# Performance work log

Measured on AMD Instinct MI355X. Metric: run time of the kernel, lower is better.

The kernel has to match this reference:

```python
import jax, jax.numpy as jnp
import numpy as np
import math
from jax import lax

B, T, C = 32, 512, 256
NL, NH, FF = 2, 4, 1024
DH = C // NH
NFREQ = 64   # n_even//2 for d_model=256 (even dims interleave sin/cos)
N_ODD = 128  # odd dims carry learned ramp a*t+b
MIN_P, MAX_P = 4.0, 10000.0


def setup_inputs() -> dict:
    key = jax.random.key(0)
    ks = jax.random.split(key, 16)
    def nrm(k, shape, s=0.02):
        return (jax.random.normal(k, shape) * s).astype(jnp.float32)
    x = jax.random.normal(ks[0], (B, T, C), jnp.float32)
    # strictly increasing normalized timestamps
    dts = jax.random.uniform(ks[1], (B, T), jnp.float32) * 0.02 + 1e-3
    ts = jnp.cumsum(dts, axis=1)
    return {
        "x": x, "ts": ts,
        "gru_Wih": nrm(ks[2], (3 * C, C)), "gru_Whh": nrm(ks[3], (3 * C, C)),
        "gru_bih": jnp.zeros((3 * C,), jnp.float32), "gru_bhh": jnp.zeros((3 * C,), jnp.float32),
        "ode_W": nrm(ks[4], (C, 4 * C)), "ode_b": jnp.zeros((C,), jnp.float32),
        "norm_ode_g": jnp.ones((C,), jnp.float32), "norm_ode_b": jnp.zeros((C,), jnp.float32),
        "norm_gru_g": jnp.ones((C,), jnp.float32), "norm_gru_b": jnp.zeros((C,), jnp.float32),
        "film_W": nrm(ks[5], (2 * C, C)), "film_b": jnp.zeros((2 * C,), jnp.float32),
        "te_a": nrm(ks[6], (N_ODD,), 1.0), "te_b": nrm(ks[7], (N_ODD,), 0.1),
        "qkv_W": nrm(ks[8], (NL, 3 * C, C)), "qkv_b": jnp.zeros((NL, 3 * C), jnp.float32),
        "out_W": nrm(ks[9], (NL, C, C)), "out_b": jnp.zeros((NL, C), jnp.float32),
        "ln1_g": jnp.ones((NL, C), jnp.float32), "ln1_b": jnp.zeros((NL, C), jnp.float32),
        "ln2_g": jnp.ones((NL, C), jnp.float32), "ln2_b": jnp.zeros((NL, C), jnp.float32),
        "ff1_W": nrm(ks[10], (NL, FF, C)), "ff1_b": jnp.zeros((NL, FF), jnp.float32),
        "ff2_W": nrm(ks[11], (NL, C, FF)), "ff2_b": jnp.zeros((NL, C), jnp.float32),
        "lnf_g": jnp.ones((C,), jnp.float32), "lnf_b": jnp.zeros((C,), jnp.float32),
    }


def _ln(x, g, b, eps=1e-5):
    m = x.mean(-1, keepdims=True)
    v = ((x - m) ** 2).mean(-1, keepdims=True)
    return (x - m) / jnp.sqrt(v + eps) * g + b


def _forward(x, ts, gru_Wih, gru_Whh, gru_bih, gru_bhh, ode_W, ode_b,
             norm_ode_g, norm_ode_b, norm_gru_g, norm_gru_b, film_W, film_b,
             te_a, te_b, qkv_W, qkv_b, out_W, out_b, ln1_g, ln1_b, ln2_g, ln2_b,
             ff1_W, ff1_b, ff2_W, ff2_b, lnf_g, lnf_b):
    Bx, Tx, Cx = x.shape

    def gru(xi, h):  # PyTorch GRUCell math
        gi = xi @ gru_Wih.T + gru_bih
        gh = h @ gru_Whh.T + gru_bhh
        ir, iz, inn = jnp.split(gi, 3, -1)
        hr, hz, hn = jnp.split(gh, 3, -1)
        r = jax.nn.sigmoid(ir + hr)
        z = jax.nn.sigmoid(iz + hz)
        n = jnp.tanh(inn + r * hn)
        return (1.0 - z) * n + z * h

    def step(h, inp):  # RK4 ODE jump + GRU jump per event
        xi, xp, dt = inp  # (B,C),(B,C),(B,1)
        dx = (xi - xp) / dt
        def f(hh):
            return jnp.tanh(jnp.concatenate([hh, xi, xp, dx], -1) @ ode_W.T + ode_b)
        k1 = f(h)
        k2 = f(h + 0.5 * dt * k1)
        k3 = f(h + 0.5 * dt * k2)
        k4 = f(h + dt * k3)
        h = h + dt / 6.0 * (k1 + 2.0 * k2 + 2.0 * k3 + k4)
        h = _ln(h, norm_ode_g, norm_ode_b)
        h = _ln(gru(xi, h), norm_gru_g, norm_gru_b)
        return h, h

    h0 = _ln(gru(x[:, 0], jnp.zeros((Bx, Cx), x.dtype)), norm_gru_g, norm_gru_b)
    xs = (x[:, 1:].swapaxes(0, 1), x[:, :-1].swapaxes(0, 1),
          (ts[:, 1:] - ts[:, :-1])[..., None].swapaxes(0, 1))
    _, ys = lax.scan(step, h0, xs)
    h = jnp.concatenate([h0[None], ys], 0).swapaxes(0, 1)  # (B,T,C)

    # FiLM params from hidden states
    gb = jax.nn.silu(h) @ film_W.T + film_b
    gamma, beta = jnp.split(gb, 2, -1)

    # TimeHybridEncoding: even dims interleaved sin/cos, odd dims learned ramp
    freqs = jnp.exp(-jnp.linspace(0.0, math.log(MAX_P / MIN_P), NFREQ)) * (2.0 * math.pi / MIN_P)
    phase = ts[..., None] * freqs  # (B,T,NFREQ)
    sc = jnp.stack([jnp.sin(phase), jnp.cos(phase)], -1).reshape(Bx, Tx, 2 * NFREQ)
    ramp = ts[..., None] * te_a + te_b  # (B,T,N_ODD)
    tme = jnp.zeros((Bx, Tx, Cx), x.dtype)
    tme = tme.at[..., 0::2].set(sc).at[..., 1::2].set(ramp)
    tme = (1.0 + gamma) * tme + beta

    # Pre-LN TransformerEncoder (eval mode: dropout off), relu FFN, final LN
    H = h + tme
    scale = 1.0 / jnp.sqrt(jnp.float32(DH))
    for l in range(NL):
        a = _ln(H, ln1_g[l], ln1_b[l])
        qkv = a @ qkv_W[l].T + qkv_b[l]
        q, k, v = jnp.split(qkv, 3, -1)
        q = q.reshape(Bx, Tx, NH, DH).transpose(0, 2, 1, 3)
        k = k.reshape(Bx, Tx, NH, DH).transpose(0, 2, 1, 3)
        v = v.reshape(Bx, Tx, NH, DH).transpose(0, 2, 1, 3)
        att = jax.nn.softmax(jnp.einsum('bhqd,bhkd->bhqk', q, k) * scale, axis=-1)
        o = jnp.einsum('bhqk,bhkd->bhqd', att, v).transpose(0, 2, 1, 3).reshape(Bx, Tx, Cx)
        H = H + o @ out_W[l].T + out_b[l]
        f2 = _ln(H, ln2_g[l], ln2_b[l])
        H = H + jax.nn.relu(f2 @ ff1_W[l].T + ff1_b[l]) @ ff2_W[l].T + ff2_b[l]
    return _ln(H, lnf_g, lnf_b)


def reference(x, ts, gru_Wih, gru_Whh, gru_bih, gru_bhh, ode_W, ode_b,
              norm_ode_g, norm_ode_b, norm_gru_g, norm_gru_b, film_W, film_b,
              te_a, te_b, qkv_W, qkv_b, out_W, out_b, ln1_g, ln1_b, ln2_g, ln2_b,
              ff1_W, ff1_b, ff2_W, ff2_b, lnf_g, lnf_b):
    return _forward(x, ts, gru_Wih, gru_Whh, gru_bih, gru_bhh, ode_W, ode_b,
                    norm_ode_g, norm_ode_b, norm_gru_g, norm_gru_b, film_W, film_b,
                    te_a, te_b, qkv_W, qkv_b, out_W, out_b, ln1_g, ln1_b, ln2_g, ln2_b,
                    ff1_W, ff1_b, ff2_W, ff2_b, lnf_g, lnf_b)
```

## Files before the change

### kernel.cpp

```cpp
#include <hip/hip_runtime.h>
#include <hip/hip_bf16.h>
#include <math.h>

typedef long long i64;

__device__ __forceinline__ float2 blockSum2_256(float a, float b, float* red) {
#pragma unroll
  for (int off = 32; off; off >>= 1) {
    a += __shfl_xor(a, off, 64);
    b += __shfl_xor(b, off, 64);
  }
  __syncthreads();
  if ((threadIdx.x & 63) == 0) {
    int w = threadIdx.x >> 6;
    red[w * 2 + 0] = a;
    red[w * 2 + 1] = b;
  }
  __syncthreads();
  return make_float2(red[0] + red[2] + red[4] + red[6],
                     red[1] + red[3] + red[5] + red[7]);
}

__device__ __forceinline__ float lnVal(float v, float g, float b, float* red) {
  float2 s = blockSum2_256(v, v * v, red);
  float mean = s.x * (1.0f / 256.0f);
  float var = s.y * (1.0f / 256.0f) - mean * mean;
  var = fmaxf(var, 0.0f);
  return (v - mean) * rsqrtf(var + 1e-5f) * g + b;
}

__device__ __forceinline__ void waveRed2d(double& a, double& b) {
#pragma unroll
  for (int off = 32; off; off >>= 1) {
    a += __shfl_xor(a, off, 64);
    b += __shfl_xor(b, off, 64);
  }
}

template <typename ACCT>
__global__ __launch_bounds__(256)
void gemm_nt_t(const float* __restrict__ A, int lda,
               const float* __restrict__ W, int ldw,
               const float* __restrict__ bias,
               const float* add,
               float* C, int ldc,
               int M, int N, int K, int relu)
{
  __shared__ float As[16][68];
  __shared__ float Ws[16][68];
  const int tid = threadIdx.x;
  const int tx = tid & 15, ty = tid >> 4;
  const int m0 = blockIdx.y * 64, n0 = blockIdx.x * 64;
  const int lrow = tid >> 2, lk = (tid & 3) << 2;
  ACCT acc[4][4] = {};
  for (int k0 = 0; k0 < K; k0 += 16) {
    float4 av = make_float4(0.f, 0.f, 0.f, 0.f);
    if (m0 + lrow < M) av = *(const float4*)(A + (i64)(m0 + lrow) * lda + k0 + lk);
    float4 wv = *(const float4*)(W + (i64)(n0 + lrow) * ldw + k0 + lk);
    As[lk + 0][lrow] = av.x; As[lk + 1][lrow] = av.y;
    As[lk + 2][lrow] = av.z; As[lk + 3][lrow] = av.w;
    Ws[lk + 0][lrow] = wv.x; Ws[lk + 1][lrow] = wv.y;
    Ws[lk + 2][lrow] = wv.z; Ws[lk + 3][lrow] = wv.w;
    __syncthreads();
#pragma unroll
    for (int kk = 0; kk < 16; ++kk) {
      ACCT a0 = (ACCT)As[kk][ty * 4 + 0], a1 = (ACCT)As[kk][ty * 4 + 1];
      ACCT a2 = (ACCT)As[kk][ty * 4 + 2], a3 = (ACCT)As[kk][ty * 4 + 3];
      ACCT b0 = (ACCT)Ws[kk][tx * 4 + 0], b1 = (ACCT)Ws[kk][tx * 4 + 1];
      ACCT b2 = (ACCT)Ws[kk][tx * 4 + 2], b3 = (ACCT)Ws[kk][tx * 4 + 3];
      acc[0][0] += a0 * b0; acc[0][1] += a0 * b1; acc[0][2] += a0 * b2; acc[0][3] += a0 * b3;
      acc[1][0] += a1 * b0; acc[1][1] += a1 * b1; acc[1][2] += a1 * b2; acc[1][3] += a1 * b3;
      acc[2][0] += a2 * b0; acc[2][1] += a2 * b1; acc[2][2] += a2 * b2; acc[2][3] += a2 * b3;
      acc[3][0] += a3 * b0; acc[3][1] += a3 * b1; acc[3][2] += a3 * b2; acc[3][3] += a3 * b3;
    }
    __syncthreads();
  }
#pragma unroll
  for (int i = 0; i < 4; ++i) {
    int m = m0 + ty * 4 + i;
    if (m >= M) continue;
#pragma unroll
    for (int j = 0; j < 4; ++j) {
      int n = n0 + tx * 4 + j;
      ACCT v = acc[i][j];
      if (bias) v += (ACCT)bias[n];
      if (relu) v = v > (ACCT)0 ? v : (ACCT)0;
      if (add) v += (ACCT)add[(i64)m * ldc + n];
      C[(i64)m * ldc + n] = (float)v;
    }
  }
}

__global__ __launch_bounds__(256)
void gemm128(const float* __restrict__ A, int lda,
             const float* __restrict__ W, int ldw,
             const float* __restrict__ bias,
             const float* add,
             float* C, int ldc,
             int K, int relu)
{
  __shared__ float As[16][132];
  __shared__ float Ws[16][132];
  const int tid = threadIdx.x;
  const int tx = tid & 15, ty = tid >> 4;
  const int m0 = blockIdx.y * 128, n0 = blockIdx.x * 128;
  const int lrow = tid >> 1;
  const int lk = (tid & 1) * 8;
  float acc[8][8] = {};
  for (int k0 = 0; k0 < K; k0 += 16) {
    const float* ap = A + (i64)(m0 + lrow) * lda + k0 + lk;
    const float* wp = W + (i64)(n0 + lrow) * ldw + k0 + lk;
    float4 av0 = *(const float4*)(ap);
    float4 av1 = *(const float4*)(ap + 4);
    float4 wv0 = *(const float4*)(wp);
    float4 wv1 = *(const float4*)(wp + 4);
    __syncthreads();
    As[lk + 0][lrow] = av0.x; As[lk + 1][lrow] = av0.y;
    As[lk + 2][lrow] = av0.z; As[lk + 3][lrow] = av0.w;
    As[lk + 4][lrow] = av1.x; As[lk + 5][lrow] = av1.y;
    As[lk + 6][lrow] = av1.z; As[lk + 7][lrow] = av1.w;
    Ws[lk + 0][lrow] = wv0.x; Ws[lk + 1][lrow] = wv0.y;
    Ws[lk + 2][lrow] = wv0.z; Ws[lk + 3][lrow] = wv0.w;
    Ws[lk + 4][lrow] = wv1.x; Ws[lk + 5][lrow] = wv1.y;
    Ws[lk + 6][lrow] = wv1.z; Ws[lk + 7][lrow] = wv1.w;
    __syncthreads();
#pragma unroll
    for (int kk = 0; kk < 16; ++kk) {
      float4 a0 = *(const float4*)&As[kk][ty * 4];
      float4 a1 = *(const float4*)&As[kk][64 + ty * 4];
      float4 b0 = *(const float4*)&Ws[kk][tx * 4];
      float4 b1 = *(const float4*)&Ws[kk][64 + tx * 4];
      float a[8] = {a0.x, a0.y, a0.z, a0.w, a1.x, a1.y, a1.z, a1.w};
      float bb[8] = {b0.x, b0.y, b0.z, b0.w, b1.x, b1.y, b1.z, b1.w};
#pragma unroll
      for (int i = 0; i < 8; ++i)
#pragma unroll
        for (int j = 0; j < 8; ++j)
          acc[i][j] = fmaf(a[i], bb[j], acc[i][j]);
    }
  }
#pragma unroll
  for (int i = 0; i < 8; ++i) {
    int m = m0 + ((i < 4) ? (ty * 4 + i) : (64 + ty * 4 + (i - 4)));
#pragma unroll
    for (int g = 0; g < 2; ++g) {
      int n = n0 + g * 64 + tx * 4;
      float v[4];
#pragma unroll
      for (int j = 0; j < 4; ++j) {
        float vv = acc[i][g * 4 + j];
        if (bias) vv += bias[n + j];
        if (relu) vv = fmaxf(vv, 0.f);
        if (add) vv += add[(i64)m * ldc + n + j];
        v[j] = vv;
      }
      *(float4*)(C + (i64)m * ldc + n) = make_float4(v[0], v[1], v[2], v[3]);
    }
  }
}

__global__ __launch_bounds__(256)
void pack_weights(const float* __restrict__ odeW, const float* __restrict__ Whh,
                  float* __restrict__ W4h, float* __restrict__ W4hh)
{
  int idx = blockIdx.x * 256 + threadIdx.x;
  if (idx < 65536) {
    int j = idx >> 8, k = idx & 255;
    W4h[((k >> 2) << 10) + (j << 2) + (k & 3)] = odeW[j * 1024 + k];
  } else {
    int t = idx - 65536;
    int j3 = t >> 8, k = t & 255;
    W4hh[(k >> 2) * 3072 + (j3 << 2) + (k & 3)] = Whh[j3 * 256 + k];
  }
}

__global__ __launch_bounds__(256)
void pack_rowsums(const float* __restrict__ odeW, const float* __restrict__ Whh,
                  const float* __restrict__ ngg, const float* __restrict__ ngb,
                  const float* __restrict__ nog, const float* __restrict__ nob,
                  double* __restrict__ Sd)
{
  int r = blockIdx.x * 256 + threadIdx.x;
  if (r < 256) {
    double s1 = 0.0, s0 = 0.0;
    for (int k = 0; k < 256; ++k) {
      double w = (double)odeW[r * 1024 + k];
      s1 += w * (double)ngg[k];
      s0 += w * (double)ngb[k];
    }
    Sd[r] = s1; Sd[256 + r] = s0;
  } else {
    int j3 = r - 256;
    double s1 = 0.0, s0 = 0.0;
    for (int k = 0; k < 256; ++k) {
      double w = (double)Whh[j3 * 256 + k];
      s1 += w * (double)nog[k];
      s0 += w * (double)nob[k];
    }
    Sd[512 + j3] = s1; Sd[1280 + j3] = s0;
  }
}

__global__ __launch_bounds__(256)
void dx_kernel(const float* __restrict__ x, const float* __restrict__ ts,
               float* __restrict__ dx)
{
  i64 row = blockIdx.x;
  int c = threadIdx.x;
  int t = (int)(row & 511);
  float v = 0.0f;
  if (t > 0) {
    double dt = (double)ts[row] - (double)ts[row - 1];
    v = (float)(((double)x[row * 256 + c] - (double)x[(row - 1) * 256 + c]) / dt);
  }
  dx[row * 256 + c] = v;
}

__global__ __launch_bounds__(256)
void silu_kernel(const float* __restrict__ in, float* __restrict__ out)
{
  i64 i = (i64)blockIdx.x * 256 + threadIdx.x;
  float v = in[i];
  out[i] = v / (1.0f + __expf(-v));
}

__global__ __launch_bounds__(256)
void fill_kernel(float* __restrict__ out, float v)
{
  i64 i = (i64)blockIdx.x * 256 + threadIdx.x;
  out[i] = v;
}

__device__ __forceinline__ float dot64s(const float* __restrict__ W, int kq, int j,
                                        const float* __restrict__ v)
{
  float a0 = 0.f, a1 = 0.f, a2 = 0.f, a3 = 0.f;
#pragma unroll
  for (int m4 = 0; m4 < 16; ++m4) {
    float4 w = *(const float4*)(W + (((kq << 4) + m4) << 10) + (j << 2));
    float4 x = *(const float4*)(v + (m4 << 2));
    a0 = fmaf(w.x, x.x, a0); a1 = fmaf(w.y, x.y, a1);
    a2 = fmaf(w.z, x.z, a2); a3 = fmaf(w.w, x.w, a3);
  }
  return (a0 + a1) + (a2 + a3);
}

__global__ __launch_bounds__(1024, 4)
void scan_kernel(const float* __restrict__ gi, const float* __restrict__ u,
                 const float* __restrict__ ts,
                 const float* __restrict__ W4h, const float* __restrict__ W4hh,
                 const double* __restrict__ Sd,
                 const float* __restrict__ bhh,
                 const float* __restrict__ nog, const float* __restrict__ nob,
                 const float* __restrict__ ngg, const float* __restrict__ ngb,
                 float* __restrict__ hseq)
{
  const int b = blockIdx.x;
  const int t = threadIdx.x;
  const int j = t & 255;
  const int kq = t >> 8;
  const int kbase = kq << 6;
  const int lane = t & 63;
  const int wv = t >> 6;

  __shared__ __align__(16) float  hraw2f[256];
  __shared__ __align__(16) double vr2[256];
  __shared__ __align__(16) float  kb[256];
  __shared__ __align__(16) float  sc_f[1024];
  __shared__ __align__(16) double predd[3][1024];
  __shared__ double redv[8];
  __shared__ double redh[8];

  const double gng = (double)ngg[j], gnb = (double)ngb[j];
  const double gog = (double)nog[j], gob = (double)nob[j];
  const double bhr = (double)bhh[j], bhz = (double)bhh[256 + j], bhn = (double)bhh[512 + j];
  const double sa1 = Sd[j], sa0 = Sd[256 + j];
  const double sg1r = Sd[512 + j],  sg0r = Sd[1280 + j];
  const double sg1z = Sd[768 + j],  sg0z = Sd[1536 + j];
  const double sg1n = Sd[1024 + j], sg0n = Sd[1792 + j];

  double hLN = 0.0, hg_raw = 0.0, mg = 0.0, invg = 1.0;

  {
    const i64 row0 = (i64)b * 512;
    if (kq == 0) {
      double ir = (double)gi[row0 * 768 + j];
      double iz = (double)gi[row0 * 768 + 256 + j];
      double inn = (double)gi[row0 * 768 + 512 + j];
      double rr = 1.0 / (1.0 + exp(-(ir + bhr)));
      double zz = 1.0 / (1.0 + exp(-(iz + bhz)));
      double nn = tanh(inn + rr * bhn);
      hg_raw = (1.0 - zz) * nn;
      hraw2f[j] = (float)(gng * hg_raw);
      double sa = hg_raw, sb = hg_raw * hg_raw;
      waveRed2d(sa, sb);
      if (lane == 0) { redh[wv * 2] = sa; redh[wv * 2 + 1] = sb; }
    }
    __syncthreads();
    if (kq == 0) {
      double S = redh[0] + redh[2] + redh[4] + redh[6];
      double Q = redh[1] + redh[3] + redh[5] + redh[7];
      mg = S * (1.0 / 256.0);
      double var = Q * (1.0 / 256.0) - mg * mg;
      var = var > 0.0 ? var : 0.0;
      invg = 1.0 / sqrt(var + 1e-5);
      hLN = (hg_raw - mg) * invg * gng + gnb;
      hseq[row0 * 256 + j] = (float)hLN;
    }
  }
  __syncthreads();

  for (int s = 0; s < 511; ++s) {
    const double dt = (double)ts[b * 512 + s + 1] - (double)ts[b * 512 + s];
    const float dtf = (float)dt;
    const i64 row = (i64)(b * 512 + s + 1);

    float u_j = 0.f, ir2f = 0.f, iz2f = 0.f, in2f = 0.f;
    if (kq == 0) {
      u_j = u[row * 256 + j];
      ir2f = gi[row * 768 + j];
      iz2f = gi[row * 768 + 256 + j];
      in2f = gi[row * 768 + 512 + j];
    }

    sc_f[t] = dot64s(W4h, kq, j, hraw2f + kbase);
    __syncthreads();
    float a_s = 0.f, k1s = 0.f, k2s = 0.f, k3s = 0.f, k4s = 0.f;
    if (kq == 0) {
      double psum = (double)(sc_f[j] + sc_f[j + 256] + sc_f[j + 512] + sc_f[j + 768]);
      double a_d = psum * invg - mg * invg * sa1 + sa0 + (double)u_j;
      a_s = (float)a_d;
      k1s = tanhf(a_s);
      kb[j] = k1s;
    }
    __syncthreads();
    sc_f[t] = dot64s(W4h, kq, j, kb + kbase);
    __syncthreads();
    if (kq == 0) {
      float bs = sc_f[j] + sc_f[j + 256] + sc_f[j + 512] + sc_f[j + 768];
      k2s = tanhf(fmaf(0.5f * dtf, bs, a_s));
      kb[j] = k2s;
    }
    __syncthreads();
    sc_f[t] = dot64s(W4h, kq, j, kb + kbase);
    __syncthreads();
    if (kq == 0) {
      float bs = sc_f[j] + sc_f[j + 256] + sc_f[j + 512] + sc_f[j + 768];
      k3s = tanhf(fmaf(0.5f * dtf, bs, a_s));
      kb[j] = k3s;
    }
    __syncthreads();
    sc_f[t] = dot64s(W4h, kq, j, kb + kbase);
    __syncthreads();
    double hode_raw = 0.0;
    if (kq == 0) {
      float bs = sc_f[j] + sc_f[j + 256] + sc_f[j + 512] + sc_f[j + 768];
      k4s = tanhf(fmaf(dtf, bs, a_s));
      hode_raw = hLN + dt * (1.0 / 6.0) *
                 ((double)k1s + 2.0 * (double)k2s + 2.0 * (double)k3s + (double)k4s);
      vr2[j] = gog * hode_raw;
      double sa = hode_raw, sb = hode_raw * hode_raw;
      waveRed2d(sa, sb);
      if (lane == 0) { redv[wv * 2] = sa; redv[wv * 2 + 1] = sb; }
    }
    __syncthreads();
    {
      double g0 = 0.0, g1 = 0.0, g2 = 0.0;
#pragma unroll 2
      for (int m4 = 0; m4 < 16; ++m4) {
        const double2* hp = (const double2*)(vr2 + kbase + (m4 << 2));
        double2 ha = hp[0], hb2 = hp[1];
        const float* base = W4hh + ((kq << 4) + m4) * 3072 + (j << 2);
        float4 w0 = *(const float4*)(base);
        float4 w1 = *(const float4*)(base + 1024);
        float4 w2 = *(const float4*)(base + 2048);
        g0 += (double)w0.x * ha.x + (double)w0.y * ha.y + (double)w0.z * hb2.x + (double)w0.w * hb2.y;
        g1 += (double)w1.x * ha.x + (double)w1.y * ha.y + (double)w1.z * hb2.x + (double)w1.w * hb2.y;
        g2 += (double)w2.x * ha.x + (double)w2.y * ha.y + (double)w2.z * hb2.x + (double)w2.w * hb2.y;
      }
      predd[0][t] = g0; predd[1][t] = g1; predd[2][t] = g2;
    }
    __syncthreads();
    if (kq == 0) {
      double mo = (redv[0] + redv[2] + redv[4] + redv[6]) * (1.0 / 256.0);
      double qo = (redv[1] + redv[3] + redv[5] + redv[7]) * (1.0 / 256.0);
      double var = qo - mo * mo; var = var > 0.0 ? var : 0.0;
      double invo = 1.0 / sqrt(var + 1e-5);
      double G0 = (predd[0][j] + predd[0][j + 256] + predd[0][j + 512] + predd[0][j + 768]) * invo
                  - mo * invo * sg1r + sg0r;
      double G1 = (predd[1][j] + predd[1][j + 256] + predd[1][j + 512] + predd[1][j + 768]) * invo
                  - mo * invo * sg1z + sg0z;
      double G2 = (predd[2][j] + predd[2][j + 256] + predd[2][j + 512] + predd[2][j + 768]) * invo
                  - mo * invo * sg1n + sg0n;
      double rr = 1.0 / (1.0 + exp(-((double)ir2f + G0 + bhr)));
      double zz = 1.0 / (1.0 + exp(-((double)iz2f + G1 + bhz)));
      double nn = tanh((double)in2f + rr * (G2 + bhn));
      double hodeLN = (hode_raw - mo) * invo * gog + gob;
      hg_raw = (1.0 - zz) * nn + zz * hodeLN;
      hraw2f[j] = (float)(gng * hg_raw);
      double sa = hg_raw, sb = hg_raw * hg_raw;
      waveRed2d(sa, sb);
      if (lane == 0) { redh[wv * 2] = sa; redh[wv * 2 + 1] = sb; }
    }
    __syncthreads();
    if (kq == 0) {
      double S = redh[0] + redh[2] + redh[4] + redh[6];
      double Q = redh[1] + redh[3] + redh[5] + redh[7];
      mg = S * (1.0 / 256.0);
      double var = Q * (1.0 / 256.0) - mg * mg;
      var = var > 0.0 ? var : 0.0;
      invg = 1.0 / sqrt(var + 1e-5);
      hLN = (hg_raw - mg) * invg * gng + gnb;
      hseq[row * 256 + j] = (float)hLN;
    }
  }
}

__global__ __launch_bounds__(256)
void tme_kernel(const float* __restrict__ hseq, const float* __restrict__ gb,
                const float* __restrict__ ts,
                const float* __restrict__ te_a, const float* __restrict__ te_b,
                float* __restrict__ H)
{
  i64 idx = (i64)blockIdx.x * 256 + threadIdx.x;
  int c = (int)(idx & 255);
  i64 bt = idx >> 8;
  double tv = (double)ts[bt];
  double tme;
  if (c & 1) {
    int i = c >> 1;
    tme = tv * (double)te_a[i] + (double)te_b[i];
  } else {
    int f = c >> 2;
    double freq = exp(-(log(2500.0) / 63.0) * (double)f) * 1.5707963267948966;
    double ph = tv * freq;
    tme = ((c >> 1) & 1) ? cos(ph) : sin(ph);
  }
  float gamma = gb[bt * 512 + c];
  float beta = gb[bt * 512 + 256 + c];
  H[idx] = hseq[idx] + (1.0f + gamma) * (float)tme + beta;
}

__global__ __launch_bounds__(256)
void ln256_f32(const float* __restrict__ in, const float* __restrict__ g,
               const float* __restrict__ b, float* __restrict__ out)
{
  __shared__ float red[8];
  i64 row = blockIdx.x;
  float v = in[row * 256 + threadIdx.x];
  out[row * 256 + threadIdx.x] = lnVal(v, g[threadIdx.x], b[threadIdx.x], red);
}

__global__ __launch_bounds__(256)
void attn_kernel(const float* __restrict__ qkv, float* __restrict__ O)
{
  __shared__ float Qs[32][68];
  __shared__ float Ks[64][68];
  __shared__ float Vs[64][68];
  int bid = blockIdx.x;
  int qb = bid & 15, bh = bid >> 4;
  int h = bh & 3, b = bh >> 2;
  int tid = threadIdx.x;
  int r = tid >> 3, dg = tid & 7;
  int lane = tid & 63;
  int q0 = qb * 32;
  i64 base = (i64)b * 512 * 768;
  {
    int rr = tid >> 3, c8 = (tid & 7) * 8;
    const float* src = qkv + base + (i64)(q0 + rr) * 768 + h * 64 + c8;
    *(float4*)&Qs[rr][c8] = *(const float4*)src;
    *(float4*)&Qs[rr][c8 + 4] = *(const float4*)(src + 4);
  }
  float m = -1e30f, l = 0.0f;
  float o[8] = {0.f, 0.f, 0.f, 0.f, 0.f, 0.f, 0.f, 0.f};
  for (int kt = 0; kt < 8; ++kt) {
    __syncthreads();
    {
      int kr = tid >> 2, c16 = (tid & 3) * 16;
      const float* srcK = qkv + base + (i64)(kt * 64 + kr) * 768 + 256 + h * 64 + c16;
      const float* srcV = srcK + 256;
#pragma unroll
      for (int ii = 0; ii < 4; ++ii) {
        *(float4*)&Ks[kr][c16 + ii * 4] = *(const float4*)(srcK + ii * 4);
        *(float4*)&Vs[kr][c16 + ii * 4] = *(const float4*)(srcV + ii * 4);
      }
    }
    __syncthreads();
    float s[8] = {0.f, 0.f, 0.f, 0.f, 0.f, 0.f, 0.f, 0.f};
#pragma unroll
    for (int d4 = 0; d4 < 16; ++d4) {
      float4 qv = *(const float4*)&Qs[r][d4 * 4];
#pragma unroll
      for (int i = 0; i < 8; ++i) {
        float4 kv = *(const float4*)&Ks[dg * 8 + i][d4 * 4];
        s[i] += qv.x * kv.x + qv.y * kv.y + qv.z * kv.z + qv.w * kv.w;
      }
    }
    float ms = -1e30f;
#pragma unroll
    for (int i = 0; i < 8; ++i) { s[i] *= 0.125f; ms = fmaxf(ms, s[i]); }
    ms = fmaxf(ms, __shfl_xor(ms, 1, 64));
    ms = fmaxf(ms, __shfl_xor(ms, 2, 64));
    ms = fmaxf(ms, __shfl_xor(ms, 4, 64));
    float mnew = fmaxf(m, ms);
    float p[8];
    float ls = 0.0f;
#pragma unroll
    for (int i = 0; i < 8; ++i) { p[i] = __expf(s[i] - mnew); ls += p[i]; }
    ls += __shfl_xor(ls, 1, 64);
    ls += __shfl_xor(ls, 2, 64);
    ls += __shfl_xor(ls, 4, 64);
    float alpha = __expf(m - mnew);
    l = l * alpha + ls;
#pragma unroll
    for (int i = 0; i < 8; ++i) o[i] *= alpha;
    m = mnew;
#pragma unroll
    for (int i = 0; i < 8; ++i) {
#pragma unroll
      for (int dgk = 0; dgk < 8; ++dgk) {
        float pv = __shfl(p[i], (lane & 56) | dgk, 64);
        int kk = dgk * 8 + i;
        float4 v0 = *(const float4*)&Vs[kk][dg * 8];
        float4 v1 = *(const float4*)&Vs[kk][dg * 8 + 4];
        o[0] += pv * v0.x; o[1] += pv * v0.y; o[2] += pv * v0.z; o[3] += pv * v0.w;
        o[4] += pv * v1.x; o[5] += pv * v1.y; o[6] += pv * v1.z; o[7] += pv * v1.w;
      }
    }
  }
  float invl = 1.0f / l;
  float* dst = O + (i64)(b * 512 + q0 + r) * 256 + h * 64 + dg * 8;
  float4 r0 = make_float4(o[0] * invl, o[1] * invl, o[2] * invl, o[3] * invl);
  float4 r1 = make_float4(o[4] * invl, o[5] * invl, o[6] * invl, o[7] * invl);
  *(float4*)dst = r0;
  *(float4*)(dst + 4) = r1;
}

extern "C" void kernel_launch(void* const* d_in, const int* in_sizes, int n_in,
                              void* d_out, int out_size, void* d_ws, size_t ws_size,
                              hipStream_t stream)
{
  (void)in_sizes; (void)n_in; (void)out_size;
  const float* x       = (const float*)d_in[0];
  const float* ts      = (const float*)d_in[1];
  const float* gru_Wih = (const float*)d_in[2];
  const float* gru_Whh = (const float*)d_in[3];
  const float* gru_bih = (const float*)d_in[4];
  const float* gru_bhh = (const float*)d_in[5];
  const float* ode_W   = (const float*)d_in[6];
  const float* ode_b   = (const float*)d_in[7];
  const float* nog     = (const float*)d_in[8];
  const float* nob     = (const float*)d_in[9];
  const float* ngg     = (const float*)d_in[10];
  const float* ngb     = (const float*)d_in[11];
  const float* film_W  = (const float*)d_in[12];
  const float* film_b  = (const float*)d_in[13];
  const float* te_a    = (const float*)d_in[14];
  const float* te_bb   = (const float*)d_in[15];
  const float* qkv_W   = (const float*)d_in[16];
  const float* qkv_b   = (const float*)d_in[17];
  const float* out_W   = (const float*)d_in[18];
  const float* out_b   = (const float*)d_in[19];
  const float* ln1_g   = (const float*)d_in[20];
  const float* ln1_b   = (const float*)d_in[21];
  const float* ln2_g   = (const float*)d_in[22];
  const float* ln2_b   = (const float*)d_in[23];
  const float* ff1_W   = (const float*)d_in[24];
  const float* ff1_b   = (const float*)d_in[25];
  const float* ff2_W   = (const float*)d_in[26];
  const float* ff2_b   = (const float*)d_in[27];
  const float* lnf_g   = (const float*)d_in[28];
  const float* lnf_b   = (const float*)d_in[29];

  const size_t NEED = 25432064ull * 4ull;
  if (ws_size < NEED) {
    fill_kernel<<<16384, 256, 0, stream>>>((float*)d_out, 1000.0f);
    return;
  }
  float*  ws   = (float*)d_ws;
  float*  W4h  = ws;
  float*  W4hh = ws + 65536;
  double* Sd   = (double*)(ws + 262144);
  float*  SA   = ws + 266240;
  float*  SB   = ws + 4460544;
  float*  Hb   = ws + 8654848;
  float*  BIG  = ws + 12849152;

  float* u = SA;  float* sh = SA;   float* aln = SA;  float* f2 = SA;
  float* dxb = SB; float* hseq = SB; float* Obuf = SB; float* ff1o = SB;
  float* gi = BIG; float* gb = BIG;  float* qkvb = BIG;

  const int MROW = 32 * 512;

  pack_weights<<<1024, 256, 0, stream>>>(ode_W, gru_Whh, W4h, W4hh);
  pack_rowsums<<<4, 256, 0, stream>>>(ode_W, gru_Whh, ngg, ngb, nog, nob, Sd);
  dx_kernel<<<MROW, 256, 0, stream>>>(x, ts, dxb);
  gemm_nt_t<double><<<dim3(12, 256), 256, 0, stream>>>(x, 256, gru_Wih, 256, gru_bih,
                                                       nullptr, gi, 768, MROW, 768, 256, 0);
  gemm_nt_t<double><<<dim3(4, 256), 256, 0, stream>>>(x + 256, 256, ode_W + 256, 1024, ode_b,
                                                      nullptr, u + 256, 256, MROW - 1, 256, 256, 0);
  gemm_nt_t<double><<<dim3(4, 256), 256, 0, stream>>>(x, 256, ode_W + 512, 1024, nullptr,
                                                      u + 256, u + 256, 256, MROW - 1, 256, 256, 0);
  gemm_nt_t<double><<<dim3(4, 256), 256, 0, stream>>>(dxb + 256, 256, ode_W + 768, 1024, nullptr,
                                                      u + 256, u + 256, 256, MROW - 1, 256, 256, 0);
  scan_kernel<<<32, 1024, 0, stream>>>(gi, u, ts, W4h, W4hh, Sd, gru_bhh,
                                       nog, nob, ngg, ngb, hseq);
  silu_kernel<<<MROW, 256, 0, stream>>>(hseq, sh);
  gemm128<<<dim3(4, 128), 256, 0, stream>>>(sh, 256, film_W, 256, film_b, nullptr,
                                            gb, 512, 256, 0);
  tme_kernel<<<MROW, 256, 0, stream>>>(hseq, gb, ts, te_a, te_bb, Hb);

  for (int l = 0; l < 2; ++l) {
    ln256_f32<<<MROW, 256, 0, stream>>>(Hb, ln1_g + 256 * l, ln1_b + 256 * l, aln);
    gemm128<<<dim3(6, 128), 256, 0, stream>>>(aln, 256, qkv_W + (i64)196608 * l, 256,
                                              qkv_b + 768 * l, nullptr,
                                              qkvb, 768, 256, 0);
    attn_kernel<<<2048, 256, 0, stream>>>(qkvb, Obuf);
    gemm128<<<dim3(2, 128), 256, 0, stream>>>(Obuf, 256, out_W + (i64)65536 * l, 256,
                                              out_b + 256 * l, Hb, Hb, 256, 256, 0);
    ln256_f32<<<MROW, 256, 0, stream>>>(Hb, ln2_g + 256 * l, ln2_b + 256 * l, f2);
    for (int c = 0; c < 4; ++c) {
      const int r0 = c * 4096;
      gemm128<<<dim3(8, 32), 256, 0, stream>>>(f2 + (i64)r0 * 256, 256,
                                               ff1_W + (i64)262144 * l, 256,
                                               ff1_b + 1024 * l, nullptr,
                                               ff1o, 1024, 256, 1);
      gemm_nt_t<float><<<dim3(4, 64), 256, 0, stream>>>(ff1o, 1024,
                                                        ff2_W + (i64)262144 * l, 1024,
                                                        ff2_b + 256 * l,
                                                        Hb + (i64)r0 * 256, Hb + (i64)r0 * 256, 256,
                                                        4096, 256, 1024, 0);
    }
  }
  ln256_f32<<<MROW, 256, 0, stream>>>(Hb, lnf_g, lnf_b, (float*)d_out);
}
```

Baseline: 9.453 ms.

## Replicate scan pointwise work across warp groups to cut barriers; fuse SiLU into GEMM

The recurrent scan kernel now has every quarter of the block redundantly compute the per-channel pointwise stages, each on its own channel subset, instead of only the first 256 threads. It double-buffers the partial-sum scratch so several __syncthreads per step can be dropped, shortening the serial critical path of the 511-step recurrence. Separately, the standalone SiLU pass before the FiLM GEMM is folded into the GEMM's A-tile load, removing one kernel and a full activation round trip. The cost is redundant transcendental work in the scan and a new per-tile branch in the GEMM.

```diff
diff --git a/kernel.cpp b/kernel.cpp
--- a/kernel.cpp
+++ b/kernel.cpp
@@ -91,13 +91,15 @@
   }
 }
 
+__device__ __forceinline__ float siluf(float v) { return v / (1.0f + __expf(-v)); }
+
 __global__ __launch_bounds__(256)
 void gemm128(const float* __restrict__ A, int lda,
              const float* __restrict__ W, int ldw,
              const float* __restrict__ bias,
              const float* add,
              float* C, int ldc,
-             int K, int relu)
+             int K, int relu, int silu_in)
 {
   __shared__ float As[16][132];
   __shared__ float Ws[16][132];
@@ -114,6 +116,10 @@
     float4 av1 = *(const float4*)(ap + 4);
     float4 wv0 = *(const float4*)(wp);
     float4 wv1 = *(const float4*)(wp + 4);
+    if (silu_in) {
+      av0.x = siluf(av0.x); av0.y = siluf(av0.y); av0.z = siluf(av0.z); av0.w = siluf(av0.w);
+      av1.x = siluf(av1.x); av1.y = siluf(av1.y); av1.z = siluf(av1.z); av1.w = siluf(av1.w);
+    }
     __syncthreads();
     As[lk + 0][lrow] = av0.x; As[lk + 1][lrow] = av0.y;
     As[lk + 2][lrow] = av0.z; As[lk + 3][lrow] = av0.w;
@@ -214,14 +220,6 @@
     v = (float)(((double)x[row * 256 + c] - (double)x[(row - 1) * 256 + c]) / dt);
   }
   dx[row * 256 + c] = v;
-}
-
-__global__ __launch_bounds__(256)
-void silu_kernel(const float* __restrict__ in, float* __restrict__ out)
-{
-  i64 i = (i64)blockIdx.x * 256 + threadIdx.x;
-  float v = in[i];
-  out[i] = v / (1.0f + __expf(-v));
 }
 
 __global__ __launch_bounds__(256)
@@ -261,109 +259,92 @@
   const int kq = t >> 8;
   const int kbase = kq << 6;
   const int lane = t & 63;
-  const int wv = t >> 6;
+  const int quad = (t >> 6) & 3;
+  const int jp = kbase | lane;
 
   __shared__ __align__(16) float  hraw2f[256];
   __shared__ __align__(16) double vr2[256];
   __shared__ __align__(16) float  kb[256];
-  __shared__ __align__(16) float  sc_f[1024];
+  __shared__ __align__(16) float  scA[1024];
+  __shared__ __align__(16) float  scB[1024];
   __shared__ __align__(16) double predd[3][1024];
   __shared__ double redv[8];
   __shared__ double redh[8];
 
-  const double gng = (double)ngg[j], gnb = (double)ngb[j];
-  const double gog = (double)nog[j], gob = (double)nob[j];
-  const double bhr = (double)bhh[j], bhz = (double)bhh[256 + j], bhn = (double)bhh[512 + j];
-  const double sa1 = Sd[j], sa0 = Sd[256 + j];
-  const double sg1r = Sd[512 + j],  sg0r = Sd[1280 + j];
-  const double sg1z = Sd[768 + j],  sg0z = Sd[1536 + j];
-  const double sg1n = Sd[1024 + j], sg0n = Sd[1792 + j];
-
-  double hLN = 0.0, hg_raw = 0.0, mg = 0.0, invg = 1.0;
+  const double gng = (double)ngg[jp], gnb = (double)ngb[jp];
+  const double gog = (double)nog[jp], gob = (double)nob[jp];
+  const double bhr = (double)bhh[jp], bhz = (double)bhh[256 + jp], bhn = (double)bhh[512 + jp];
+  const double sa1 = Sd[jp], sa0 = Sd[256 + jp];
+  const double sg1r = Sd[512 + jp],  sg0r = Sd[1280 + jp];
+  const double sg1z = Sd[768 + jp],  sg0z = Sd[1536 + jp];
+  const double sg1n = Sd[1024 + jp], sg0n = Sd[1792 + jp];
+
+  double hLN = 0.0, mg = 0.0, invg = 1.0;
 
   {
     const i64 row0 = (i64)b * 512;
-    if (kq == 0) {
-      double ir = (double)gi[row0 * 768 + j];
-      double iz = (double)gi[row0 * 768 + 256 + j];
-      double inn = (double)gi[row0 * 768 + 512 + j];
-      double rr = 1.0 / (1.0 + exp(-(ir + bhr)));
-      double zz = 1.0 / (1.0 + exp(-(iz + bhz)));
-      double nn = tanh(inn + rr * bhn);
-      hg_raw = (1.0 - zz) * nn;
-      hraw2f[j] = (float)(gng * hg_raw);
-      double sa = hg_raw, sb = hg_raw * hg_raw;
-      waveRed2d(sa, sb);
-      if (lane == 0) { redh[wv * 2] = sa; redh[wv * 2 + 1] = sb; }
-    }
-    __syncthreads();
-    if (kq == 0) {
-      double S = redh[0] + redh[2] + redh[4] + redh[6];
-      double Q = redh[1] + redh[3] + redh[5] + redh[7];
-      mg = S * (1.0 / 256.0);
-      double var = Q * (1.0 / 256.0) - mg * mg;
-      var = var > 0.0 ? var : 0.0;
-      invg = 1.0 / sqrt(var + 1e-5);
-      hLN = (hg_raw - mg) * invg * gng + gnb;
-      hseq[row0 * 256 + j] = (float)hLN;
-    }
-  }
-  __syncthreads();
+    double ir = (double)gi[row0 * 768 + jp];
+    double iz = (double)gi[row0 * 768 + 256 + jp];
+    double inn = (double)gi[row0 * 768 + 512 + jp];
+    double rr = 1.0 / (1.0 + exp(-(ir + bhr)));
+    double zz = 1.0 / (1.0 + exp(-(iz + bhz)));
+    double nn = tanh(inn + rr * bhn);
+    double hg_raw = (1.0 - zz) * nn;
+    hraw2f[jp] = (float)(gng * hg_raw);
+    double sa = hg_raw, sb = hg_raw * hg_raw;
+    waveRed2d(sa, sb);
+    if (lane == 0 && quad == 0) { redh[kq * 2] = sa; redh[kq * 2 + 1] = sb; }
+    __syncthreads();
+    double S = redh[0] + redh[2] + redh[4] + redh[6];
+    double Q = redh[1] + redh[3] + redh[5] + redh[7];
+    mg = S * (1.0 / 256.0);
+    double var = Q * (1.0 / 256.0) - mg * mg;
+    var = var > 0.0 ? var : 0.0;
+    invg = 1.0 / sqrt(var + 1e-5);
+    hLN = (hg_raw - mg) * invg * gng + gnb;
+    if (quad == 0) hseq[row0 * 256 + jp] = (float)hLN;
+    __syncthreads();
+  }
 
   for (int s = 0; s < 511; ++s) {
     const double dt = (double)ts[b * 512 + s + 1] - (double)ts[b * 512 + s];
     const float dtf = (float)dt;
     const i64 row = (i64)(b * 512 + s + 1);
 
-    float u_j = 0.f, ir2f = 0.f, iz2f = 0.f, in2f = 0.f;
-    if (kq == 0) {
-      u_j = u[row * 256 + j];
-      ir2f = gi[row * 768 + j];
-      iz2f = gi[row * 768 + 256 + j];
-      in2f = gi[row * 768 + 512 + j];
-    }
-
-    sc_f[t] = dot64s(W4h, kq, j, hraw2f + kbase);
-    __syncthreads();
-    float a_s = 0.f, k1s = 0.f, k2s = 0.f, k3s = 0.f, k4s = 0.f;
-    if (kq == 0) {
-      double psum = (double)(sc_f[j] + sc_f[j + 256] + sc_f[j + 512] + sc_f[j + 768]);
-      double a_d = psum * invg - mg * invg * sa1 + sa0 + (double)u_j;
-      a_s = (float)a_d;
-      k1s = tanhf(a_s);
-      kb[j] = k1s;
-    }
-    __syncthreads();
-    sc_f[t] = dot64s(W4h, kq, j, kb + kbase);
-    __syncthreads();
-    if (kq == 0) {
-      float bs = sc_f[j] + sc_f[j + 256] + sc_f[j + 512] + sc_f[j + 768];
-      k2s = tanhf(fmaf(0.5f * dtf, bs, a_s));
-      kb[j] = k2s;
-    }
-    __syncthreads();
-    sc_f[t] = dot64s(W4h, kq, j, kb + kbase);
-    __syncthreads();
-    if (kq == 0) {
-      float bs = sc_f[j] + sc_f[j + 256] + sc_f[j + 512] + sc_f[j + 768];
-      k3s = tanhf(fmaf(0.5f * dtf, bs, a_s));
-      kb[j] = k3s;
-    }
-    __syncthreads();
-    sc_f[t] = dot64s(W4h, kq, j, kb + kbase);
-    __syncthreads();
-    double hode_raw = 0.0;
-    if (kq == 0) {
-      float bs = sc_f[j] + sc_f[j + 256] + sc_f[j + 512] + sc_f[j + 768];
-      k4s = tanhf(fmaf(dtf, bs, a_s));
-      hode_raw = hLN + dt * (1.0 / 6.0) *
-                 ((double)k1s + 2.0 * (double)k2s + 2.0 * (double)k3s + (double)k4s);
-      vr2[j] = gog * hode_raw;
+    const float u_j  = u[row * 256 + jp];
+    const float ir2f = gi[row * 768 + jp];
+    const float iz2f = gi[row * 768 + 256 + jp];
+    const float in2f = gi[row * 768 + 512 + jp];
+
+    scA[t] = dot64s(W4h, kq, j, hraw2f + kbase);
+    __syncthreads();
+    double psum = (double)(scA[jp] + scA[jp + 256] + scA[jp + 512] + scA[jp + 768]);
+    double a_d = psum * invg - mg * invg * sa1 + sa0 + (double)u_j;
+    float a_s = (float)a_d;
+    float k1s = tanhf(a_s);
+    kb[jp] = k1s;
+    scB[t] = dot64s(W4h, kq, j, kb + kbase);
+    __syncthreads();
+    float bs2 = scB[jp] + scB[jp + 256] + scB[jp + 512] + scB[jp + 768];
+    float k2s = tanhf(fmaf(0.5f * dtf, bs2, a_s));
+    kb[jp] = k2s;
+    scA[t] = dot64s(W4h, kq, j, kb + kbase);
+    __syncthreads();
+    float bs3 = scA[jp] + scA[jp + 256] + scA[jp + 512] + scA[jp + 768];
+    float k3s = tanhf(fmaf(0.5f * dtf, bs3, a_s));
+    kb[jp] = k3s;
+    scB[t] = dot64s(W4h, kq, j, kb + kbase);
+    __syncthreads();
+    float bs4 = scB[jp] + scB[jp + 256] + scB[jp + 512] + scB[jp + 768];
+    float k4s = tanhf(fmaf(dtf, bs4, a_s));
+    double hode_raw = hLN + dt * (1.0 / 6.0) *
+                      ((double)k1s + 2.0 * (double)k2s + 2.0 * (double)k3s + (double)k4s);
+    vr2[jp] = gog * hode_raw;
+    {
       double sa = hode_raw, sb = hode_raw * hode_raw;
       waveRed2d(sa, sb);
-      if (lane == 0) { redv[wv * 2] = sa; redv[wv * 2 + 1] = sb; }
-    }
-    __syncthreads();
+      if (lane == 0 && quad == 0) { redv[kq * 2] = sa; redv[kq * 2 + 1] = sb; }
+    }
     {
       double g0 = 0.0, g1 = 0.0, g2 = 0.0;
 #pragma unroll 2
@@ -381,29 +362,30 @@
       predd[0][t] = g0; predd[1][t] = g1; predd[2][t] = g2;
     }
     __syncthreads();
-    if (kq == 0) {
+    double hg_raw;
+    {
       double mo = (redv[0] + redv[2] + redv[4] + redv[6]) * (1.0 / 256.0);
       double qo = (redv[1] + redv[3] + redv[5] + redv[7]) * (1.0 / 256.0);
       double var = qo - mo * mo; var = var > 0.0 ? var : 0.0;
       double invo = 1.0 / sqrt(var + 1e-5);
-      double G0 = (predd[0][j] + predd[0][j + 256] + predd[0][j + 512] + predd[0][j + 768]) * invo
+      double G0 = (predd[0][jp] + predd[0][jp + 256] + predd[0][jp + 512] + predd[0][jp + 768]) * invo
                   - mo * invo * sg1r + sg0r;
-      double G1 = (predd[1][j] + predd[1][j + 256] + predd[1][j + 512] + predd[1][j + 768]) * invo
+      double G1 = (predd[1][jp] + predd[1][jp + 256] + predd[1][jp + 512] + predd[1][jp + 768]) * invo
                   - mo * invo * sg1z + sg0z;
-      double G2 = (predd[2][j] + predd[2][j + 256] + predd[2][j + 512] + predd[2][j + 768]) * invo
+      double G2 = (predd[2][jp] + predd[2][jp + 256] + predd[2][jp + 512] + predd[2][jp + 768]) * invo
                   - mo * invo * sg1n + sg0n;
       double rr = 1.0 / (1.0 + exp(-((double)ir2f + G0 + bhr)));
       double zz = 1.0 / (1.0 + exp(-((double)iz2f + G1 + bhz)));
       double nn = tanh((double)in2f + rr * (G2 + bhn));
       double hodeLN = (hode_raw - mo) * invo * gog + gob;
       hg_raw = (1.0 - zz) * nn + zz * hodeLN;
-      hraw2f[j] = (float)(gng * hg_raw);
+      hraw2f[jp] = (float)(gng * hg_raw);
       double sa = hg_raw, sb = hg_raw * hg_raw;
       waveRed2d(sa, sb);
-      if (lane == 0) { redh[wv * 2] = sa; redh[wv * 2 + 1] = sb; }
-    }
-    __syncthreads();
-    if (kq == 0) {
+      if (lane == 0 && quad == 0) { redh[kq * 2] = sa; redh[kq * 2 + 1] = sb; }
+    }
+    __syncthreads();
+    {
       double S = redh[0] + redh[2] + redh[4] + redh[6];
       double Q = redh[1] + redh[3] + redh[5] + redh[7];
       mg = S * (1.0 / 256.0);
@@ -411,7 +393,7 @@
       var = var > 0.0 ? var : 0.0;
       invg = 1.0 / sqrt(var + 1e-5);
       hLN = (hg_raw - mg) * invg * gng + gnb;
-      hseq[row * 256 + j] = (float)hLN;
+      if (quad == 0) hseq[row * 256 + jp] = (float)hLN;
     }
   }
 }
@@ -586,7 +568,7 @@
   float*  Hb   = ws + 8654848;
   float*  BIG  = ws + 12849152;
 
-  float* u = SA;  float* sh = SA;   float* aln = SA;  float* f2 = SA;
+  float* u = SA;   float* aln = SA;  float* f2 = SA;
   float* dxb = SB; float* hseq = SB; float* Obuf = SB; float* ff1o = SB;
   float* gi = BIG; float* gb = BIG;  float* qkvb = BIG;
 
@@ -605,26 +587,25 @@
                                                       u + 256, u + 256, 256, MROW - 1, 256, 256, 0);
   scan_kernel<<<32, 1024, 0, stream>>>(gi, u, ts, W4h, W4hh, Sd, gru_bhh,
                                        nog, nob, ngg, ngb, hseq);
-  silu_kernel<<<MROW, 256, 0, stream>>>(hseq, sh);
-  gemm128<<<dim3(4, 128), 256, 0, stream>>>(sh, 256, film_W, 256, film_b, nullptr,
-                                            gb, 512, 256, 0);
+  gemm128<<<dim3(4, 128), 256, 0, stream>>>(hseq, 256, film_W, 256, film_b, nullptr,
+                                            gb, 512, 256, 0, 1);
   tme_kernel<<<MROW, 256, 0, stream>>>(hseq, gb, ts, te_a, te_bb, Hb);
 
   for (int l = 0; l < 2; ++l) {
     ln256_f32<<<MROW, 256, 0, stream>>>(Hb, ln1_g + 256 * l, ln1_b + 256 * l, aln);
     gemm128<<<dim3(6, 128), 256, 0, stream>>>(aln, 256, qkv_W + (i64)196608 * l, 256,
                                               qkv_b + 768 * l, nullptr,
-                                              qkvb, 768, 256, 0);
+                                              qkvb, 768, 256, 0, 0);
     attn_kernel<<<2048, 256, 0, stream>>>(qkvb, Obuf);
     gemm128<<<dim3(2, 128), 256, 0, stream>>>(Obuf, 256, out_W + (i64)65536 * l, 256,
-                                              out_b + 256 * l, Hb, Hb, 256, 256, 0);
+                                              out_b + 256 * l, Hb, Hb, 256, 256, 0, 0);
     ln256_f32<<<MROW, 256, 0, stream>>>(Hb, ln2_g + 256 * l, ln2_b + 256 * l, f2);
     for (int c = 0; c < 4; ++c) {
       const int r0 = c * 4096;
       gemm128<<<dim3(8, 32), 256, 0, stream>>>(f2 + (i64)r0 * 256, 256,
                                                ff1_W + (i64)262144 * l, 256,
                                                ff1_b + 1024 * l, nullptr,
-                                               ff1o, 1024, 256, 1);
+                                               ff1o, 1024, 256, 1, 0);
       gemm_nt_t<float><<<dim3(4, 64), 256, 0, stream>>>(ff1o, 1024,
                                                         ff2_W + (i64)262144 * l, 1024,
                                                         ff2_b + 256 * l,
```

New measurement: 10.61 ms. 1.12x slower.
